# Optimization experiments

Hardware: AMD Instinct MI355X
Metric: run time of the kernel (lower is better)

Reference implementation:

```python
import jax, jax.numpy as jnp
import numpy as np

B, S, D_IN, D_OUT = 4, 2048, 1024, 1024

def setup_inputs() -> dict:
    key = jax.random.key(0)
    k_x, k_q, k_k, k_v = jax.random.split(key, 4)
    return {
        "x": jax.random.normal(k_x, (B, S, D_IN), dtype=jnp.float32),
        "W_query": jax.random.uniform(k_q, (D_IN, D_OUT), dtype=jnp.float32),
        "W_key": jax.random.uniform(k_k, (D_IN, D_OUT), dtype=jnp.float32),
        "W_value": jax.random.uniform(k_v, (D_IN, D_OUT), dtype=jnp.float32),
    }

def reference(x, W_query, W_key, W_value):
    seq_len = x.shape[1]
    d_out = W_key.shape[-1]
    # fused QKV projection: x @ concat([Wq, Wk, Wv], -1), then split
    qkv = x @ jnp.concatenate([W_query, W_key, W_value], axis=-1)  # [B,S,3*d_out]
    query, key, value = jnp.split(qkv, 3, axis=2)
    # raw scores [B,S,S]; causal mask applied BEFORE scaling (as in source)
    attn_weights = jnp.einsum("bqd,bkd->bqk", query, key)
    causal = jnp.triu(jnp.ones((seq_len, seq_len), dtype=bool), k=1)
    attn_weights = jnp.where(causal[None, :, :], -jnp.inf, attn_weights)
    scaled = attn_weights / jnp.asarray(d_out, x.dtype) ** 0.5
    attn_scores = jax.nn.softmax(scaled, axis=-1)  # dropout p=0 -> identity
    context_vectors = jnp.einsum("bqk,bkd->bqd", attn_scores, value)
    return (context_vectors, attn_scores)
```

## Files before the change

kernel.cpp:

```cpp
#include <hip/hip_runtime.h>
#include <cstdint>
#include <cstddef>


#define S_LEN 2048
#define D_DIM 1024
#define NBATCH 4
#define MEG (1024 * 1024)

typedef __attribute__((ext_vector_type(4))) float floatx4;
typedef __attribute__((ext_vector_type(8))) __bf16 bf16x8;
typedef __attribute__((ext_vector_type(8))) short short8v;

__device__ __forceinline__ unsigned short f2bf(float f) {
  union { float f; unsigned u; } v; v.f = f;
  unsigned r = v.u + 0x7FFF + ((v.u >> 16) & 1);
  return (unsigned short)(r >> 16);
}
__device__ __forceinline__ float bf2f(unsigned short h) {
  union { unsigned u; float f; } v; v.u = ((unsigned)h) << 16; return v.f;
}

__device__ __forceinline__ void async_copy16(const void* g, void* l) {
  __builtin_amdgcn_global_load_lds(
      (const __attribute__((address_space(1))) void*)g,
      (__attribute__((address_space(3))) void*)l, 16, 0, 0);
}

#define VMCNT0() asm volatile("s_waitcnt vmcnt(0)" ::: "memory")
#define RAW_BAR() __builtin_amdgcn_s_barrier()
#define MFMA_BF16 __builtin_amdgcn_mfma_f32_16x16x32_bf16


__device__ __forceinline__ void split_core8(
    const short* __restrict__ Ah, const short* __restrict__ Al,
    const short* __restrict__ Bh, const short* __restrict__ Bl,
    int lda, int ldb, int kIters, int blockM, int blockN,
    short (*AsH)[256][32], short (*AsL)[256][32],
    short (*BsH)[128][32], short (*BsL)[128][32],
    floatx4 (&acc)[4][4])
{
  const int tid  = threadIdx.x;
  const int lane = tid & 63;
  const int wave = tid >> 6;
  const int wm = (wave >> 1) * 64;
  const int wn = (wave & 1) * 64;
  const int fm = lane & 15;
  const int fu = lane >> 4;

  int rA[4], sA[4], rB[4], sB[4];
  #pragma unroll
  for (int i = 0; i < 4; ++i) {
    rA[i] = wm + i * 16 + fm;
    sA[i] = (fu ^ ((rA[i] >> 1) & 3)) * 8;
    rB[i] = wn + i * 16 + fm;
    sB[i] = (fu ^ ((rB[i] >> 1) & 3)) * 8;
  }

  floatx4 zero = {0.f, 0.f, 0.f, 0.f};
  #pragma unroll
  for (int i = 0; i < 4; ++i)
    #pragma unroll
    for (int j = 0; j < 4; ++j)
      acc[i][j] = zero;

  const int r0 = tid >> 2;
  const int u0 = tid & 3;
  const int su = (u0 ^ ((r0 >> 1) & 3)) * 8;
  const size_t a0 = (size_t)(blockM + r0) * lda + su;
  const size_t a1 = a0 + (size_t)128 * lda;
  const size_t b0 = (size_t)(blockN + r0) * ldb + su;

  auto stage0 = [&](int bf, int kb) {
    async_copy16(Ah + a0 + kb, &AsH[bf][r0][u0 * 8]);
    async_copy16(Al + a0 + kb, &AsL[bf][r0][u0 * 8]);
    async_copy16(Bh + b0 + kb, &BsH[bf][r0][u0 * 8]);
  };
  auto stage1 = [&](int bf, int kb) {
    async_copy16(Ah + a1 + kb, &AsH[bf][r0 + 128][u0 * 8]);
    async_copy16(Al + a1 + kb, &AsL[bf][r0 + 128][u0 * 8]);
    async_copy16(Bl + b0 + kb, &BsL[bf][r0][u0 * 8]);
  };

  stage0(0, 0);
  stage1(0, 0);
  VMCNT0();
  RAW_BAR();

  for (int kt = 0; kt < kIters; ++kt) {
    const int cur = kt & 1;
    const int kb = (kt + 1) * 32;
    const bool pf = (kt + 1) < kIters;

    bf16x8 bh[4], bl[4];
    #pragma unroll
    for (int j = 0; j < 4; ++j) {
      bh[j] = *(const bf16x8*)(&BsH[cur][rB[j]][sB[j]]);
      bl[j] = *(const bf16x8*)(&BsL[cur][rB[j]][sB[j]]);
    }
    bf16x8 ah0 = *(const bf16x8*)(&AsH[cur][rA[0]][sA[0]]);
    bf16x8 al0 = *(const bf16x8*)(&AsL[cur][rA[0]][sA[0]]);
    bf16x8 ah1 = *(const bf16x8*)(&AsH[cur][rA[1]][sA[1]]);
    bf16x8 al1 = *(const bf16x8*)(&AsL[cur][rA[1]][sA[1]]);
    if (pf) stage0(cur ^ 1, kb);
    RAW_BAR();
    __builtin_amdgcn_s_setprio(1);
    #pragma unroll
    for (int j = 0; j < 4; ++j) {
      acc[0][j] = MFMA_BF16(ah0, bh[j], acc[0][j], 0, 0, 0);
      acc[0][j] = MFMA_BF16(ah0, bl[j], acc[0][j], 0, 0, 0);
      acc[0][j] = MFMA_BF16(al0, bh[j], acc[0][j], 0, 0, 0);
      acc[1][j] = MFMA_BF16(ah1, bh[j], acc[1][j], 0, 0, 0);
      acc[1][j] = MFMA_BF16(ah1, bl[j], acc[1][j], 0, 0, 0);
      acc[1][j] = MFMA_BF16(al1, bh[j], acc[1][j], 0, 0, 0);
    }
    __builtin_amdgcn_s_setprio(0);
    RAW_BAR();

    bf16x8 ah2 = *(const bf16x8*)(&AsH[cur][rA[2]][sA[2]]);
    bf16x8 al2 = *(const bf16x8*)(&AsL[cur][rA[2]][sA[2]]);
    bf16x8 ah3 = *(const bf16x8*)(&AsH[cur][rA[3]][sA[3]]);
    bf16x8 al3 = *(const bf16x8*)(&AsL[cur][rA[3]][sA[3]]);
    if (pf) stage1(cur ^ 1, kb);
    RAW_BAR();
    __builtin_amdgcn_s_setprio(1);
    #pragma unroll
    for (int j = 0; j < 4; ++j) {
      acc[2][j] = MFMA_BF16(ah2, bh[j], acc[2][j], 0, 0, 0);
      acc[2][j] = MFMA_BF16(ah2, bl[j], acc[2][j], 0, 0, 0);
      acc[2][j] = MFMA_BF16(al2, bh[j], acc[2][j], 0, 0, 0);
      acc[3][j] = MFMA_BF16(ah3, bh[j], acc[3][j], 0, 0, 0);
      acc[3][j] = MFMA_BF16(ah3, bl[j], acc[3][j], 0, 0, 0);
      acc[3][j] = MFMA_BF16(al3, bh[j], acc[3][j], 0, 0, 0);
    }
    __builtin_amdgcn_s_setprio(0);
    VMCNT0();
    RAW_BAR();
  }
}

__device__ __forceinline__ void single_core8(
    const short* __restrict__ A, const short* __restrict__ B,
    int lda, int ldb, int kIters, int blockM, int blockN,
    short (*As)[256][32], short (*Bs)[128][32], floatx4 (&acc)[4][4])
{
  const int tid  = threadIdx.x;
  const int lane = tid & 63;
  const int wave = tid >> 6;
  const int wm = (wave >> 1) * 64;
  const int wn = (wave & 1) * 64;
  const int fm = lane & 15;
  const int fu = lane >> 4;

  int rA[4], sA[4], rB[4], sB[4];
  #pragma unroll
  for (int i = 0; i < 4; ++i) {
    rA[i] = wm + i * 16 + fm;
    sA[i] = (fu ^ ((rA[i] >> 1) & 3)) * 8;
    rB[i] = wn + i * 16 + fm;
    sB[i] = (fu ^ ((rB[i] >> 1) & 3)) * 8;
  }

  floatx4 zero = {0.f, 0.f, 0.f, 0.f};
  #pragma unroll
  for (int i = 0; i < 4; ++i)
    #pragma unroll
    for (int j = 0; j < 4; ++j)
      acc[i][j] = zero;

  const int r0 = tid >> 2;
  const int u0 = tid & 3;
  const int su = (u0 ^ ((r0 >> 1) & 3)) * 8;
  const size_t a0 = (size_t)(blockM + r0) * lda + su;
  const size_t a1 = a0 + (size_t)128 * lda;
  const size_t b0 = (size_t)(blockN + r0) * ldb + su;

  auto stage0 = [&](int bf, int kb) {
    async_copy16(A + a0 + kb, &As[bf][r0][u0 * 8]);
    async_copy16(B + b0 + kb, &Bs[bf][r0][u0 * 8]);
  };
  auto stage1 = [&](int bf, int kb) {
    async_copy16(A + a1 + kb, &As[bf][r0 + 128][u0 * 8]);
  };

  stage0(0, 0);
  stage1(0, 0);
  VMCNT0();
  RAW_BAR();

  for (int kt = 0; kt < kIters; ++kt) {
    const int cur = kt & 1;
    const int kb = (kt + 1) * 32;
    const bool pf = (kt + 1) < kIters;

    bf16x8 bfr[4];
    #pragma unroll
    for (int j = 0; j < 4; ++j)
      bfr[j] = *(const bf16x8*)(&Bs[cur][rB[j]][sB[j]]);
    bf16x8 a0f = *(const bf16x8*)(&As[cur][rA[0]][sA[0]]);
    bf16x8 a1f = *(const bf16x8*)(&As[cur][rA[1]][sA[1]]);
    if (pf) stage0(cur ^ 1, kb);
    RAW_BAR();
    __builtin_amdgcn_s_setprio(1);
    #pragma unroll
    for (int j = 0; j < 4; ++j) {
      acc[0][j] = MFMA_BF16(a0f, bfr[j], acc[0][j], 0, 0, 0);
      acc[1][j] = MFMA_BF16(a1f, bfr[j], acc[1][j], 0, 0, 0);
    }
    __builtin_amdgcn_s_setprio(0);
    RAW_BAR();

    bf16x8 a2f = *(const bf16x8*)(&As[cur][rA[2]][sA[2]]);
    bf16x8 a3f = *(const bf16x8*)(&As[cur][rA[3]][sA[3]]);
    if (pf) stage1(cur ^ 1, kb);
    RAW_BAR();
    __builtin_amdgcn_s_setprio(1);
    #pragma unroll
    for (int j = 0; j < 4; ++j) {
      acc[2][j] = MFMA_BF16(a2f, bfr[j], acc[2][j], 0, 0, 0);
      acc[3][j] = MFMA_BF16(a3f, bfr[j], acc[3][j], 0, 0, 0);
    }
    __builtin_amdgcn_s_setprio(0);
    VMCNT0();
    RAW_BAR();
  }
}


__global__ __launch_bounds__(256) void k_cvt_w(
    const float* __restrict__ wq, const float* __restrict__ wk,
    const float* __restrict__ wv,
    short* __restrict__ wqh, short* __restrict__ wql,
    short* __restrict__ wkh, short* __restrict__ wkl,
    short* __restrict__ wvt, float* __restrict__ muSum)
{
  const int bid = blockIdx.x;
  const int tid = threadIdx.x;
  if (bid < 1024) {
    const float4* src;
    short *dh, *dl;
    size_t idx;
    if (bid < 512) {
      idx = (size_t)bid * 256 + tid;
      src = (const float4*)wq; dh = wqh; dl = wql;
    } else {
      idx = (size_t)(bid - 512) * 256 + tid;
      src = (const float4*)wk; dh = wkh; dl = wkl;
    }
    const float4 u4 = src[idx * 2];
    const float4 w4 = src[idx * 2 + 1];
    float f[8] = {u4.x, u4.y, u4.z, u4.w, w4.x, w4.y, w4.z, w4.w};
    short8v oh, ol;
    #pragma unroll
    for (int e = 0; e < 8; ++e) {
      const unsigned short h = f2bf(f[e]);
      oh[e] = (short)h;
      ol[e] = (short)f2bf(f[e] - bf2f(h));
    }
    *(short8v*)(dh + idx * 8) = oh;
    *(short8v*)(dl + idx * 8) = ol;
  } else {
    if (bid == 1024) {
      float4 z = {0.f, 0.f, 0.f, 0.f};
      ((float4*)muSum)[tid] = z;
    }
    const int rem = bid - 1024;
    const int bx = rem & 31, by = rem >> 5;
    const int tx = tid & 31, ty = tid >> 5;
    __shared__ float tile[32][33];
    const int colIn = bx * 32 + tx;
    #pragma unroll
    for (int i = 0; i < 4; ++i) {
      const int rowIn = by * 32 + ty + i * 8;
      tile[ty + i * 8][tx] = wv[(size_t)rowIn * D_DIM + colIn];
    }
    __syncthreads();
    const int colOut = by * 32 + tx;
    #pragma unroll
    for (int i = 0; i < 4; ++i) {
      const int rowOut = bx * 32 + ty + i * 8;
      wvt[(size_t)rowOut * D_DIM + colOut] = (short)f2bf(tile[tx][ty + i * 8]);
    }
  }
}


__global__ __launch_bounds__(256) void k_m_cvtx(
    const short* __restrict__ wqh, const short* __restrict__ wql,
    const short* __restrict__ wkh, const short* __restrict__ wkl,
    short* __restrict__ mth, short* __restrict__ mtl,
    float* __restrict__ muSum,
    const float4* __restrict__ x,
    short* __restrict__ xh, short* __restrict__ xl)
{
  __shared__ alignas(16) short AsH[2][64][32];
  __shared__ alignas(16) short AsL[2][64][32];
  __shared__ alignas(16) short BsH[2][64][32];
  __shared__ alignas(16) short BsL[2][64][32];
  const int g = blockIdx.x;
  const int tid = threadIdx.x;

  if (g < 256) {
    floatx4 acc[2][2];
    const int blockM = (g >> 4) * 64;
    const int blockN = (g & 15) * 64;
    const int lane = tid & 63, wave = tid >> 6;
    const int wm = (wave >> 1) * 32, wn = (wave & 1) * 32;
    const int fm = lane & 15, fk = (lane >> 4) * 8;

    floatx4 zero = {0.f, 0.f, 0.f, 0.f};
    #pragma unroll
    for (int i = 0; i < 2; ++i)
      #pragma unroll
      for (int j = 0; j < 2; ++j)
        acc[i][j] = zero;

    const int sr = tid >> 2;
    const int sc = (tid & 3) * 8;
    const short* ah0 = wkh + (size_t)(blockM + sr) * D_DIM + sc;
    const short* al0 = wkl + (size_t)(blockM + sr) * D_DIM + sc;
    const short* bh0 = wqh + (size_t)(blockN + sr) * D_DIM + sc;
    const short* bl0 = wql + (size_t)(blockN + sr) * D_DIM + sc;
    short* ahB = &AsH[0][0][0]; short* alB = &AsL[0][0][0];
    short* bhB = &BsH[0][0][0]; short* blB = &BsL[0][0][0];
    const int l0 = tid * 8, l1 = (tid + 256) * 8;

    for (int kt = 0; kt < 16; ++kt) {
      const int kb = kt * 64;
      async_copy16(ah0 + kb, ahB + l0);
      async_copy16(ah0 + kb + 32, ahB + l1);
      async_copy16(al0 + kb, alB + l0);
      async_copy16(al0 + kb + 32, alB + l1);
      async_copy16(bh0 + kb, bhB + l0);
      async_copy16(bh0 + kb + 32, bhB + l1);
      async_copy16(bl0 + kb, blB + l0);
      async_copy16(bl0 + kb + 32, blB + l1);
      __syncthreads();
      #pragma unroll
      for (int ks = 0; ks < 2; ++ks) {
        bf16x8 ah[2], al[2], bh[2], bl[2];
        #pragma unroll
        for (int i = 0; i < 2; ++i) {
          ah[i] = *(const bf16x8*)(&AsH[ks][wm + i * 16 + fm][fk]);
          al[i] = *(const bf16x8*)(&AsL[ks][wm + i * 16 + fm][fk]);
        }
        #pragma unroll
        for (int j = 0; j < 2; ++j) {
          bh[j] = *(const bf16x8*)(&BsH[ks][wn + j * 16 + fm][fk]);
          bl[j] = *(const bf16x8*)(&BsL[ks][wn + j * 16 + fm][fk]);
        }
        #pragma unroll
        for (int i = 0; i < 2; ++i)
          #pragma unroll
          for (int j = 0; j < 2; ++j) {
            acc[i][j] = MFMA_BF16(ah[i], bh[j], acc[i][j], 0, 0, 0);
            acc[i][j] = MFMA_BF16(ah[i], bl[j], acc[i][j], 0, 0, 0);
            acc[i][j] = MFMA_BF16(al[i], bh[j], acc[i][j], 0, 0, 0);
          }
      }
      __syncthreads();
    }

    const int rb = wm + ((lane >> 4) << 2);
    const int cb = wn + (lane & 15);
    #pragma unroll
    for (int i = 0; i < 2; ++i)
      #pragma unroll
      for (int j = 0; j < 2; ++j) {
        const int n = blockN + cb + j * 16;
        #pragma unroll
        for (int r = 0; r < 2 * 2; ++r) {
          const int m = blockM + rb + i * 16 + r;
          const float f = acc[i][j][r];
          const unsigned short h = f2bf(f);
          mth[(size_t)m * D_DIM + n] = (short)h;
          mtl[(size_t)m * D_DIM + n] = (short)f2bf(f - bf2f(h));
        }
      }
    #pragma unroll
    for (int i = 0; i < 2; ++i)
      #pragma unroll
      for (int r = 0; r < 4; ++r) {
        float v = acc[i][0][r] + acc[i][1][r];
        v += __shfl_xor(v, 1); v += __shfl_xor(v, 2);
        v += __shfl_xor(v, 4); v += __shfl_xor(v, 8);
        if ((lane & 15) == 0)
          atomicAdd(&muSum[blockM + rb + i * 16 + r], v);
      }
  } else {
    const size_t idx = (size_t)(g - 256) * 256 + tid;
    const float4 u4 = x[idx * 2];
    const float4 w4 = x[idx * 2 + 1];
    float f[8] = {u4.x, u4.y, u4.z, u4.w, w4.x, w4.y, w4.z, w4.w};
    short8v oh, ol;
    #pragma unroll
    for (int e = 0; e < 8; ++e) {
      const unsigned short h = f2bf(f[e]);
      oh[e] = (short)h;
      ol[e] = (short)f2bf(f[e] - bf2f(h));
    }
    *(short8v*)(xh + idx * 8) = oh;
    *(short8v*)(xl + idx * 8) = ol;
  }
}


__global__ __launch_bounds__(256) void k_rowstats(
    const short* __restrict__ xh, const short* __restrict__ xl,
    const float* __restrict__ muSum, float* __restrict__ sq, float* __restrict__ u)
{
  const int r = blockIdx.x, tid = threadIdx.x;
  const ushort4 h = *(const ushort4*)(xh + (size_t)r * D_DIM + tid * 4);
  const ushort4 l = *(const ushort4*)(xl + (size_t)r * D_DIM + tid * 4);
  const float4 m4 = *(const float4*)(muSum + tid * 4);
  const float x0 = bf2f(h.x) + bf2f(l.x);
  const float x1 = bf2f(h.y) + bf2f(l.y);
  const float x2 = bf2f(h.z) + bf2f(l.z);
  const float x3 = bf2f(h.w) + bf2f(l.w);
  float s = x0 + x1 + x2 + x3;
  float uu = m4.x * x0 + m4.y * x1 + m4.z * x2 + m4.w * x3;
  #pragma unroll
  for (int off = 32; off > 0; off >>= 1) {
    s  += __shfl_xor(s, off);
    uu += __shfl_xor(uu, off);
  }
  __shared__ float ps[4], pu[4];
  if ((tid & 63) == 0) { ps[tid >> 6] = s; pu[tid >> 6] = uu; }
  __syncthreads();
  if (tid == 0) {
    sq[r] = ps[0] + ps[1] + ps[2] + ps[3];
    u[r]  = (pu[0] + pu[1] + pu[2] + pu[3]) * (1.0f / 1024.0f);
  }
}


__global__ __launch_bounds__(512) void k_gemm_n8(
    const short* __restrict__ xh, const short* __restrict__ xl,
    const short* __restrict__ mth, const short* __restrict__ mtl,
    const float* __restrict__ sq, const float* __restrict__ muSum,
    short* __restrict__ nh, short* __restrict__ nl)
{
  __shared__ alignas(16) short AsH[2][256][32];
  __shared__ alignas(16) short AsL[2][256][32];
  __shared__ alignas(16) short BsH[2][128][32];
  __shared__ alignas(16) short BsL[2][128][32];
  floatx4 acc[4][4];
  const int g = blockIdx.x;
  const int swz = (g & 7) * 32 + (g >> 3);
  const int blockM = (swz >> 3) * 256;
  const int blockN = (swz & 7) * 128;
  split_core8(xh, xl, mth, mtl, D_DIM, D_DIM, D_DIM / 32,
              blockM, blockN, AsH, AsL, BsH, BsL, acc);

  const int tid = threadIdx.x, lane = tid & 63, wave = tid >> 6;
  const int wm = (wave >> 1) * 64, wn = (wave & 1) * 64;
  const int rb = wm + ((lane >> 4) << 2);
  const int cb = wn + (lane & 15);
  #pragma unroll
  for (int i = 0; i < 4; ++i)
    #pragma unroll
    for (int j = 0; j < 4; ++j) {
      const int n = blockN + cb + j * 16;
      const float muv = muSum[n] * (1.0f / 1024.0f);
      #pragma unroll
      for (int r = 0; r < 4; ++r) {
        const int m = blockM + rb + i * 16 + r;
        const float f = acc[i][j][r] - sq[m] * muv;
        const unsigned short h = f2bf(f);
        nh[(size_t)m * D_DIM + n] = (short)h;
        nl[(size_t)m * D_DIM + n] = (short)f2bf(f - bf2f(h));
      }
    }
}


__global__ __launch_bounds__(512) void k_gemm_sv8(
    const short* __restrict__ nh, const short* __restrict__ nl,
    const short* __restrict__ xh, const short* __restrict__ xl,
    const float* __restrict__ sq, const float* __restrict__ u,
    const short* __restrict__ wvt, float* __restrict__ attn,
    short* __restrict__ vt)
{
  __shared__ alignas(16) short AsH[2][256][32];
  __shared__ alignas(16) short AsL[2][256][32];
  __shared__ alignas(16) short BsH[2][128][32];
  __shared__ alignas(16) short BsL[2][128][32];
  floatx4 acc[4][4];

  const int g = blockIdx.x;
  const int tid = threadIdx.x, lane = tid & 63, wave = tid >> 6;
  const int wm = (wave >> 1) * 64, wn = (wave & 1) * 64;
  const int rb = wm + ((lane >> 4) << 2);
  const int cb = wn + (lane & 15);

  if (g < 288) {
    const int item = (g & 7) * 36 + (g >> 3);
    const int b = item / 72;
    int t = item - b * 72;
    int bi = 0;
    while (t >= 2 * bi + 2) { t -= 2 * bi + 2; ++bi; }
    const int bj = t;

    const size_t boff = (size_t)b * S_LEN * D_DIM;
    split_core8(nh + boff, nl + boff, xh + boff, xl + boff,
                D_DIM, D_DIM, D_DIM / 32, bi * 256, bj * 128,
                AsH, AsL, BsH, BsL, acc);

    float* out = attn + (size_t)b * S_LEN * S_LEN;
    const int rowBase = (b << 11) + bi * 256;
    const int colBase = (b << 11) + bj * 128;
    #pragma unroll
    for (int j = 0; j < 4; ++j) {
      const int n = bj * 128 + cb + j * 16;
      const float uv = u[colBase + cb + j * 16];
      #pragma unroll
      for (int i = 0; i < 4; ++i)
        #pragma unroll
        for (int r = 0; r < 4; ++r) {
          const int m = bi * 256 + rb + i * 16 + r;
          const float sv = sq[rowBase + rb + i * 16 + r];
          out[(size_t)m * S_LEN + n] = acc[i][j][r] + sv * uv;
        }
    }
  } else {
    const int vb = g - 288;
    const int blockM = (vb >> 3) * 256;
    const int blockN = (vb & 7) * 128;
    single_core8(xh, wvt, D_DIM, D_DIM, D_DIM / 32, blockM, blockN,
                 AsH, BsH, acc);
    #pragma unroll
    for (int i = 0; i < 4; ++i)
      #pragma unroll
      for (int j = 0; j < 4; ++j) {
        const int n = blockN + cb + j * 16;
        const int m0 = blockM + rb + i * 16;
        const int b = m0 >> 11;
        const int s0 = m0 & (S_LEN - 1);
        ushort4 pk;
        pk.x = f2bf(acc[i][j][0]); pk.y = f2bf(acc[i][j][1]);
        pk.z = f2bf(acc[i][j][2]); pk.w = f2bf(acc[i][j][3]);
        *(ushort4*)(vt + ((size_t)b * D_DIM + n) * S_LEN + s0) = pk;
      }
  }
}


__global__ __launch_bounds__(256) void k_softmax(float* __restrict__ attn,
                                                 short* __restrict__ pb) {
  const int b = blockIdx.x >> 11;
  const int q = blockIdx.x & (S_LEN - 1);
  float* row  = attn + ((size_t)b * S_LEN + q) * S_LEN;
  short* prow = pb   + ((size_t)b * S_LEN + q) * S_LEN;
  const int tid = threadIdx.x;
  const int k0 = tid * 8;
  const int kBand = ((q >> 7) + 1) << 7;
  __shared__ float sMax[4], sSum[4];

  float v[8];
  if (k0 <= q) {
    const float4 a0 = *(const float4*)(row + k0);
    const float4 a1 = *(const float4*)(row + k0 + 4);
    v[0] = a0.x; v[1] = a0.y; v[2] = a0.z; v[3] = a0.w;
    v[4] = a1.x; v[5] = a1.y; v[6] = a1.z; v[7] = a1.w;
  } else {
    #pragma unroll
    for (int e = 0; e < 8; ++e) v[e] = -3.0e38f;
  }

  float mx = -3.0e38f;
  #pragma unroll
  for (int e = 0; e < 8; ++e) {
    v[e] = (k0 + e <= q) ? v[e] : -3.0e38f;
    mx = fmaxf(mx, v[e]);
  }
  #pragma unroll
  for (int off = 32; off > 0; off >>= 1) mx = fmaxf(mx, __shfl_xor(mx, off));
  if ((tid & 63) == 0) sMax[tid >> 6] = mx;
  __syncthreads();
  mx = fmaxf(fmaxf(sMax[0], sMax[1]), fmaxf(sMax[2], sMax[3]));

  float s = 0.f;
  #pragma unroll
  for (int e = 0; e < 8; ++e) {
    const float p = (k0 + e <= q) ? __expf((v[e] - mx) * 0.03125f) : 0.f;
    v[e] = p;
    s += p;
  }
  #pragma unroll
  for (int off = 32; off > 0; off >>= 1) s += __shfl_xor(s, off);
  if ((tid & 63) == 0) sSum[tid >> 6] = s;
  __syncthreads();
  s = sSum[0] + sSum[1] + sSum[2] + sSum[3];
  const float inv = 1.0f / s;

  float o[8];
  #pragma unroll
  for (int e = 0; e < 8; ++e) o[e] = v[e] * inv;
  float4 w0 = {o[0], o[1], o[2], o[3]};
  float4 w1 = {o[4], o[5], o[6], o[7]};
  *(float4*)(row + k0) = w0;
  *(float4*)(row + k0 + 4) = w1;
  if (k0 < kBand) {
    ushort4 p0, p1;
    p0.x = f2bf(o[0]); p0.y = f2bf(o[1]); p0.z = f2bf(o[2]); p0.w = f2bf(o[3]);
    p1.x = f2bf(o[4]); p1.y = f2bf(o[5]); p1.z = f2bf(o[6]); p1.w = f2bf(o[7]);
    *(ushort4*)(prow + k0) = p0;
    *(ushort4*)(prow + k0 + 4) = p1;
  }
}


__global__ __launch_bounds__(256) void k_gemm_ctx(
    const short* __restrict__ pb, const short* __restrict__ vt,
    float* __restrict__ ctx)
{
  __shared__ alignas(16) short As2[2][128][32];
  __shared__ alignas(16) short Bs2[2][128][32];
  floatx4 acc[4][4];
  const int b = blockIdx.z;
  const int by = 15 - blockIdx.y;
  const int blockM = by * 128;
  const int blockN = blockIdx.x * 128;
  const int kIters = (by + 1) * 2;
  const short* A = pb + (size_t)b * S_LEN * S_LEN;
  const short* B = vt + (size_t)b * D_DIM * S_LEN;

  const int tid = threadIdx.x, lane = tid & 63, wave = tid >> 6;
  const int wm = (wave >> 1) * 64, wn = (wave & 1) * 64;
  const int fm = lane & 15, fk = (lane >> 4) * 8;
  const int r0 = tid >> 2, c0 = (tid & 3) * 8;

  floatx4 zero = {0.f, 0.f, 0.f, 0.f};
  #pragma unroll
  for (int i = 0; i < 4; ++i)
    #pragma unroll
    for (int j = 0; j < 4; ++j)
      acc[i][j] = zero;

  const short* a0 = A + (size_t)(blockM + r0) * S_LEN + c0;
  const short* a1 = a0 + (size_t)64 * S_LEN;
  const short* b0 = B + (size_t)(blockN + r0) * S_LEN + c0;
  const short* b1 = b0 + (size_t)64 * S_LEN;
  short* asBase = &As2[0][0][0];
  short* bsBase = &Bs2[0][0][0];
  short* as0 = asBase + (size_t)tid * 8;
  short* as1 = asBase + (size_t)(tid + 256) * 8;
  short* as2 = asBase + (size_t)(tid + 512) * 8;
  short* as3 = asBase + (size_t)(tid + 768) * 8;
  short* bs0 = bsBase + (size_t)tid * 8;
  short* bs1 = bsBase + (size_t)(tid + 256) * 8;
  short* bs2 = bsBase + (size_t)(tid + 512) * 8;
  short* bs3 = bsBase + (size_t)(tid + 768) * 8;

  for (int kt = 0; kt < kIters; ++kt) {
    const int kb = kt * 64;
    async_copy16(a0 + kb, as0);
    async_copy16(a1 + kb, as1);
    async_copy16(a0 + kb + 32, as2);
    async_copy16(a1 + kb + 32, as3);
    async_copy16(b0 + kb, bs0);
    async_copy16(b1 + kb, bs1);
    async_copy16(b0 + kb + 32, bs2);
    async_copy16(b1 + kb + 32, bs3);
    __syncthreads();
    #pragma unroll
    for (int ks = 0; ks < 2; ++ks) {
      bf16x8 af[4], bfr[4];
      #pragma unroll
      for (int i = 0; i < 4; ++i)
        af[i] = *(const bf16x8*)(&As2[ks][wm + i * 16 + fm][fk]);
      #pragma unroll
      for (int j = 0; j < 4; ++j)
        bfr[j] = *(const bf16x8*)(&Bs2[ks][wn + j * 16 + fm][fk]);
      #pragma unroll
      for (int i = 0; i < 4; ++i)
        #pragma unroll
        for (int j = 0; j < 4; ++j)
          acc[i][j] = MFMA_BF16(af[i], bfr[j], acc[i][j], 0, 0, 0);
    }
    __syncthreads();
  }

  float* out = ctx + (size_t)b * S_LEN * D_DIM;
  const int rb = wm + ((lane >> 4) << 2);
  const int cb = wn + (lane & 15);
  #pragma unroll
  for (int i = 0; i < 4; ++i)
    #pragma unroll
    for (int j = 0; j < 4; ++j) {
      const int n = blockN + cb + j * 16;
      #pragma unroll
      for (int r = 0; r < 4; ++r) {
        const int m = blockM + rb + i * 16 + r;
        out[(size_t)m * D_DIM + n] = acc[i][j][r];
      }
    }
}


extern "C" void kernel_launch(void* const* d_in, const int* in_sizes, int n_in,
                              void* d_out, int out_size, void* d_ws, size_t ws_size,
                              hipStream_t stream) {
  const float* x  = (const float*)d_in[0];
  const float* wq = (const float*)d_in[1];
  const float* wk = (const float*)d_in[2];
  const float* wv = (const float*)d_in[3];

  float* out  = (float*)d_out;
  float* ctx  = out;
  float* attn = out + (size_t)NBATCH * S_LEN * D_DIM;

  short* ws  = (short*)d_ws;
  short* xh  = ws;
  short* xl  = xh + (size_t)8 * MEG;
  short* wqh = xl + (size_t)8 * MEG;
  short* wql = wqh + (size_t)1 * MEG;
  short* wkh = wql + (size_t)1 * MEG;
  short* wkl = wkh + (size_t)1 * MEG;
  short* wvt = wkl + (size_t)1 * MEG;
  short* mth = wvt + (size_t)1 * MEG;
  short* mtl = mth + (size_t)1 * MEG;
  short* nh  = mtl + (size_t)1 * MEG;
  short* nl  = nh + (size_t)8 * MEG;
  short* vt  = nl + (size_t)8 * MEG;
  short* pb  = nh;
  float* fb  = (float*)(vt + (size_t)8 * MEG);
  float* muS = fb;
  float* sq  = fb + 1024;
  float* u   = sq + 8192;

  k_cvt_w<<<2048, 256, 0, stream>>>(wq, wk, wv, wqh, wql, wkh, wkl, wvt, muS);
  k_m_cvtx<<<4352, 256, 0, stream>>>(wqh, wql, wkh, wkl, mth, mtl, muS,
                                     (const float4*)x, xh, xl);
  k_rowstats<<<8192, 256, 0, stream>>>(xh, xl, muS, sq, u);
  k_gemm_n8<<<256, 512, 0, stream>>>(xh, xl, mth, mtl, sq, muS, nh, nl);
  k_gemm_sv8<<<544, 512, 0, stream>>>(nh, nl, xh, xl, sq, u, wvt, attn, vt);
  k_softmax<<<NBATCH * S_LEN, 256, 0, stream>>>(attn, pb);
  k_gemm_ctx<<<dim3(8, 16, 4), 256, 0, stream>>>(pb, vt, ctx);
}
```

Baseline: 366.2 us.

## Triple-buffer LDS tiles in GEMM cores with prefetch depth two

Both GEMM core loops (split and single precision) move from double to triple buffering. Two k-tiles are prefetched ahead, and the end-of-iteration wait becomes a partial vmcnt wait instead of draining all global-to-LDS loads. The goal is to hide more global memory latency behind the MFMA work. In exchange, LDS use per block rises by half in the split kernels. Any other caller of single_core8 whose buffers are not resized to three would index out of bounds.

```diff
diff --git a/kernel.cpp b/kernel.cpp
--- a/kernel.cpp
+++ b/kernel.cpp
@@ -28,6 +28,8 @@
 }
 
 #define VMCNT0() asm volatile("s_waitcnt vmcnt(0)" ::: "memory")
+#define VMCNT3() asm volatile("s_waitcnt vmcnt(3)" ::: "memory")
+#define VMCNT6() asm volatile("s_waitcnt vmcnt(6)" ::: "memory")
 #define RAW_BAR() __builtin_amdgcn_s_barrier()
 #define MFMA_BF16 __builtin_amdgcn_mfma_f32_16x16x32_bf16
 
@@ -84,13 +86,17 @@
 
   stage0(0, 0);
   stage1(0, 0);
-  VMCNT0();
+  stage0(1, 32);
+  stage1(1, 32);
+  VMCNT6();
   RAW_BAR();
 
+  int cur = 0;
   for (int kt = 0; kt < kIters; ++kt) {
-    const int cur = kt & 1;
-    const int kb = (kt + 1) * 32;
-    const bool pf = (kt + 1) < kIters;
+    const int pf2 = kt + 2;
+    const bool pf = pf2 < kIters;
+    const int pbuf = cur >= 1 ? cur - 1 : 2;
+    const int kb = pf2 * 32;
 
     bf16x8 bh[4], bl[4];
     #pragma unroll
@@ -102,7 +108,7 @@
     bf16x8 al0 = *(const bf16x8*)(&AsL[cur][rA[0]][sA[0]]);
     bf16x8 ah1 = *(const bf16x8*)(&AsH[cur][rA[1]][sA[1]]);
     bf16x8 al1 = *(const bf16x8*)(&AsL[cur][rA[1]][sA[1]]);
-    if (pf) stage0(cur ^ 1, kb);
+    if (pf) stage0(pbuf, kb);
     RAW_BAR();
     __builtin_amdgcn_s_setprio(1);
     #pragma unroll
@@ -121,7 +127,7 @@
     bf16x8 al2 = *(const bf16x8*)(&AsL[cur][rA[2]][sA[2]]);
     bf16x8 ah3 = *(const bf16x8*)(&AsH[cur][rA[3]][sA[3]]);
     bf16x8 al3 = *(const bf16x8*)(&AsL[cur][rA[3]][sA[3]]);
-    if (pf) stage1(cur ^ 1, kb);
+    if (pf) stage1(pbuf, kb);
     RAW_BAR();
     __builtin_amdgcn_s_setprio(1);
     #pragma unroll
@@ -134,8 +140,9 @@
       acc[3][j] = MFMA_BF16(al3, bh[j], acc[3][j], 0, 0, 0);
     }
     __builtin_amdgcn_s_setprio(0);
-    VMCNT0();
+    if (pf) { VMCNT6(); } else { VMCNT0(); }
     RAW_BAR();
+    cur = (cur == 2) ? 0 : cur + 1;
   }
 }
 
@@ -185,13 +192,17 @@
 
   stage0(0, 0);
   stage1(0, 0);
-  VMCNT0();
+  stage0(1, 32);
+  stage1(1, 32);
+  VMCNT3();
   RAW_BAR();
 
+  int cur = 0;
   for (int kt = 0; kt < kIters; ++kt) {
-    const int cur = kt & 1;
-    const int kb = (kt + 1) * 32;
-    const bool pf = (kt + 1) < kIters;
+    const int pf2 = kt + 2;
+    const bool pf = pf2 < kIters;
+    const int pbuf = cur >= 1 ? cur - 1 : 2;
+    const int kb = pf2 * 32;
 
     bf16x8 bfr[4];
     #pragma unroll
@@ -199,7 +210,7 @@
       bfr[j] = *(const bf16x8*)(&Bs[cur][rB[j]][sB[j]]);
     bf16x8 a0f = *(const bf16x8*)(&As[cur][rA[0]][sA[0]]);
     bf16x8 a1f = *(const bf16x8*)(&As[cur][rA[1]][sA[1]]);
-    if (pf) stage0(cur ^ 1, kb);
+    if (pf) stage0(pbuf, kb);
     RAW_BAR();
     __builtin_amdgcn_s_setprio(1);
     #pragma unroll
@@ -212,7 +223,7 @@
 
     bf16x8 a2f = *(const bf16x8*)(&As[cur][rA[2]][sA[2]]);
     bf16x8 a3f = *(const bf16x8*)(&As[cur][rA[3]][sA[3]]);
-    if (pf) stage1(cur ^ 1, kb);
+    if (pf) stage1(pbuf, kb);
     RAW_BAR();
     __builtin_amdgcn_s_setprio(1);
     #pragma unroll
@@ -221,8 +232,9 @@
       acc[3][j] = MFMA_BF16(a3f, bfr[j], acc[3][j], 0, 0, 0);
     }
     __builtin_amdgcn_s_setprio(0);
-    VMCNT0();
+    if (pf) { VMCNT3(); } else { VMCNT0(); }
     RAW_BAR();
+    cur = (cur == 2) ? 0 : cur + 1;
   }
 }
 
@@ -440,10 +452,10 @@
     const float* __restrict__ sq, const float* __restrict__ muSum,
     short* __restrict__ nh, short* __restrict__ nl)
 {
-  __shared__ alignas(16) short AsH[2][256][32];
-  __shared__ alignas(16) short AsL[2][256][32];
-  __shared__ alignas(16) short BsH[2][128][32];
-  __shared__ alignas(16) short BsL[2][128][32];
+  __shared__ alignas(16) short AsH[3][256][32];
+  __shared__ alignas(16) short AsL[3][256][32];
+  __shared__ alignas(16) short BsH[3][128][32];
+  __shared__ alignas(16) short BsL[3][128][32];
   floatx4 acc[4][4];
   const int g = blockIdx.x;
   const int swz = (g & 7) * 32 + (g >> 3);
@@ -481,10 +493,10 @@
     const short* __restrict__ wvt, float* __restrict__ attn,
     short* __restrict__ vt)
 {
-  __shared__ alignas(16) short AsH[2][256][32];
-  __shared__ alignas(16) short AsL[2][256][32];
-  __shared__ alignas(16) short BsH[2][128][32];
-  __shared__ alignas(16) short BsL[2][128][32];
+  __shared__ alignas(16) short AsH[3][256][32];
+  __shared__ alignas(16) short AsL[3][256][32];
+  __shared__ alignas(16) short BsH[3][128][32];
+  __shared__ alignas(16) short BsL[3][128][32];
   floatx4 acc[4][4];
 
   const int g = blockIdx.x;
```

Result: no change. 367.9 us (+0.5%).

## Restructure GEMM cores into register-double-buffered pipeline with one barrier per k-step

Applied to the files above, without the earlier changes.

Both GEMM inner loops now prefetch two k-tiles ahead into LDS and preload the next tile's fragments into a second register set while the current tile's MFMAs run. This cuts the barriers per iteration from four to one and overlaps LDS reads with matrix math. In exchange it doubles fragment register usage, which may lower occupancy or cause spills. The loop is unrolled by two and assumes an even kIters, and the prefetch into buffer kt&1 relies on that buffer's fragments already having been read into registers before the barrier.

```diff
diff --git a/kernel.cpp b/kernel.cpp
--- a/kernel.cpp
+++ b/kernel.cpp
@@ -28,6 +28,9 @@
 }
 
 #define VMCNT0() asm volatile("s_waitcnt vmcnt(0)" ::: "memory")
+#define VMCNT6() asm volatile("s_waitcnt vmcnt(6)" ::: "memory")
+#define VMCNT3() asm volatile("s_waitcnt vmcnt(3)" ::: "memory")
+#define LGKM0()  asm volatile("s_waitcnt lgkmcnt(0)" ::: "memory")
 #define RAW_BAR() __builtin_amdgcn_s_barrier()
 #define MFMA_BF16 __builtin_amdgcn_mfma_f32_16x16x32_bf16
 
@@ -71,71 +74,67 @@
   const size_t a1 = a0 + (size_t)128 * lda;
   const size_t b0 = (size_t)(blockN + r0) * ldb + su;
 
-  auto stage0 = [&](int bf, int kb) {
+  auto stage = [&](int bf, int kb) {
     async_copy16(Ah + a0 + kb, &AsH[bf][r0][u0 * 8]);
     async_copy16(Al + a0 + kb, &AsL[bf][r0][u0 * 8]);
     async_copy16(Bh + b0 + kb, &BsH[bf][r0][u0 * 8]);
-  };
-  auto stage1 = [&](int bf, int kb) {
     async_copy16(Ah + a1 + kb, &AsH[bf][r0 + 128][u0 * 8]);
     async_copy16(Al + a1 + kb, &AsL[bf][r0 + 128][u0 * 8]);
     async_copy16(Bl + b0 + kb, &BsL[bf][r0][u0 * 8]);
   };
 
-  stage0(0, 0);
-  stage1(0, 0);
+  bf16x8 A0h[4], A0l[4], B0h[4], B0l[4];
+  bf16x8 A1h[4], A1l[4], B1h[4], B1l[4];
+
+  stage(0, 0);
+  stage(1, 32);
+  VMCNT6();
+  RAW_BAR();
+  #pragma unroll
+  for (int j = 0; j < 4; ++j) {
+    B0h[j] = *(const bf16x8*)(&BsH[0][rB[j]][sB[j]]);
+    B0l[j] = *(const bf16x8*)(&BsL[0][rB[j]][sB[j]]);
+    A0h[j] = *(const bf16x8*)(&AsH[0][rA[j]][sA[j]]);
+    A0l[j] = *(const bf16x8*)(&AsL[0][rA[j]][sA[j]]);
+  }
+  LGKM0();
   VMCNT0();
   RAW_BAR();
 
-  for (int kt = 0; kt < kIters; ++kt) {
-    const int cur = kt & 1;
-    const int kb = (kt + 1) * 32;
-    const bool pf = (kt + 1) < kIters;
-
-    bf16x8 bh[4], bl[4];
-    #pragma unroll
-    for (int j = 0; j < 4; ++j) {
-      bh[j] = *(const bf16x8*)(&BsH[cur][rB[j]][sB[j]]);
-      bl[j] = *(const bf16x8*)(&BsL[cur][rB[j]][sB[j]]);
-    }
-    bf16x8 ah0 = *(const bf16x8*)(&AsH[cur][rA[0]][sA[0]]);
-    bf16x8 al0 = *(const bf16x8*)(&AsL[cur][rA[0]][sA[0]]);
-    bf16x8 ah1 = *(const bf16x8*)(&AsH[cur][rA[1]][sA[1]]);
-    bf16x8 al1 = *(const bf16x8*)(&AsL[cur][rA[1]][sA[1]]);
-    if (pf) stage0(cur ^ 1, kb);
-    RAW_BAR();
+  auto iterf = [&](int kt,
+                   bf16x8 (&cAh)[4], bf16x8 (&cAl)[4],
+                   bf16x8 (&cBh)[4], bf16x8 (&cBl)[4],
+                   bf16x8 (&nAh)[4], bf16x8 (&nAl)[4],
+                   bf16x8 (&nBh)[4], bf16x8 (&nBl)[4]) {
+    const int nbuf = (kt + 1) & 1;
+    if (kt + 2 < kIters) stage(kt & 1, (kt + 2) * 32);
+    if (kt + 1 < kIters) {
+      #pragma unroll
+      for (int j = 0; j < 4; ++j) {
+        nBh[j] = *(const bf16x8*)(&BsH[nbuf][rB[j]][sB[j]]);
+        nBl[j] = *(const bf16x8*)(&BsL[nbuf][rB[j]][sB[j]]);
+        nAh[j] = *(const bf16x8*)(&AsH[nbuf][rA[j]][sA[j]]);
+        nAl[j] = *(const bf16x8*)(&AsL[nbuf][rA[j]][sA[j]]);
+      }
+    }
     __builtin_amdgcn_s_setprio(1);
     #pragma unroll
-    for (int j = 0; j < 4; ++j) {
-      acc[0][j] = MFMA_BF16(ah0, bh[j], acc[0][j], 0, 0, 0);
-      acc[0][j] = MFMA_BF16(ah0, bl[j], acc[0][j], 0, 0, 0);
-      acc[0][j] = MFMA_BF16(al0, bh[j], acc[0][j], 0, 0, 0);
-      acc[1][j] = MFMA_BF16(ah1, bh[j], acc[1][j], 0, 0, 0);
-      acc[1][j] = MFMA_BF16(ah1, bl[j], acc[1][j], 0, 0, 0);
-      acc[1][j] = MFMA_BF16(al1, bh[j], acc[1][j], 0, 0, 0);
-    }
+    for (int i = 0; i < 4; ++i)
+      #pragma unroll
+      for (int j = 0; j < 4; ++j) {
+        acc[i][j] = MFMA_BF16(cAh[i], cBh[j], acc[i][j], 0, 0, 0);
+        acc[i][j] = MFMA_BF16(cAh[i], cBl[j], acc[i][j], 0, 0, 0);
+        acc[i][j] = MFMA_BF16(cAl[i], cBh[j], acc[i][j], 0, 0, 0);
+      }
     __builtin_amdgcn_s_setprio(0);
-    RAW_BAR();
-
-    bf16x8 ah2 = *(const bf16x8*)(&AsH[cur][rA[2]][sA[2]]);
-    bf16x8 al2 = *(const bf16x8*)(&AsL[cur][rA[2]][sA[2]]);
-    bf16x8 ah3 = *(const bf16x8*)(&AsH[cur][rA[3]][sA[3]]);
-    bf16x8 al3 = *(const bf16x8*)(&AsL[cur][rA[3]][sA[3]]);
-    if (pf) stage1(cur ^ 1, kb);
-    RAW_BAR();
-    __builtin_amdgcn_s_setprio(1);
-    #pragma unroll
-    for (int j = 0; j < 4; ++j) {
-      acc[2][j] = MFMA_BF16(ah2, bh[j], acc[2][j], 0, 0, 0);
-      acc[2][j] = MFMA_BF16(ah2, bl[j], acc[2][j], 0, 0, 0);
-      acc[2][j] = MFMA_BF16(al2, bh[j], acc[2][j], 0, 0, 0);
-      acc[3][j] = MFMA_BF16(ah3, bh[j], acc[3][j], 0, 0, 0);
-      acc[3][j] = MFMA_BF16(ah3, bl[j], acc[3][j], 0, 0, 0);
-      acc[3][j] = MFMA_BF16(al3, bh[j], acc[3][j], 0, 0, 0);
-    }
-    __builtin_amdgcn_s_setprio(0);
+    LGKM0();
     VMCNT0();
     RAW_BAR();
+  };
+
+  for (int kt = 0; kt < kIters; kt += 2) {
+    iterf(kt,     A0h, A0l, B0h, B0l, A1h, A1l, B1h, B1l);
+    iterf(kt + 1, A1h, A1l, B1h, B1l, A0h, A0l, B0h, B0l);
   }
 }
 
@@ -175,54 +174,54 @@
   const size_t a1 = a0 + (size_t)128 * lda;
   const size_t b0 = (size_t)(blockN + r0) * ldb + su;
 
-  auto stage0 = [&](int bf, int kb) {
+  auto stage = [&](int bf, int kb) {
     async_copy16(A + a0 + kb, &As[bf][r0][u0 * 8]);
     async_copy16(B + b0 + kb, &Bs[bf][r0][u0 * 8]);
-  };
-  auto stage1 = [&](int bf, int kb) {
     async_copy16(A + a1 + kb, &As[bf][r0 + 128][u0 * 8]);
   };
 
-  stage0(0, 0);
-  stage1(0, 0);
+  bf16x8 A0f[4], B0f[4], A1f[4], B1f[4];
+
+  stage(0, 0);
+  stage(1, 32);
+  VMCNT3();
+  RAW_BAR();
+  #pragma unroll
+  for (int j = 0; j < 4; ++j) {
+    B0f[j] = *(const bf16x8*)(&Bs[0][rB[j]][sB[j]]);
+    A0f[j] = *(const bf16x8*)(&As[0][rA[j]][sA[j]]);
+  }
+  LGKM0();
   VMCNT0();
   RAW_BAR();
 
-  for (int kt = 0; kt < kIters; ++kt) {
-    const int cur = kt & 1;
-    const int kb = (kt + 1) * 32;
-    const bool pf = (kt + 1) < kIters;
-
-    bf16x8 bfr[4];
-    #pragma unroll
-    for (int j = 0; j < 4; ++j)
-      bfr[j] = *(const bf16x8*)(&Bs[cur][rB[j]][sB[j]]);
-    bf16x8 a0f = *(const bf16x8*)(&As[cur][rA[0]][sA[0]]);
-    bf16x8 a1f = *(const bf16x8*)(&As[cur][rA[1]][sA[1]]);
-    if (pf) stage0(cur ^ 1, kb);
-    RAW_BAR();
+  auto iterf = [&](int kt,
+                   bf16x8 (&cAf)[4], bf16x8 (&cBf)[4],
+                   bf16x8 (&nAf)[4], bf16x8 (&nBf)[4]) {
+    const int nbuf = (kt + 1) & 1;
+    if (kt + 2 < kIters) stage(kt & 1, (kt + 2) * 32);
+    if (kt + 1 < kIters) {
+      #pragma unroll
+      for (int j = 0; j < 4; ++j) {
+        nBf[j] = *(const bf16x8*)(&Bs[nbuf][rB[j]][sB[j]]);
+        nAf[j] = *(const bf16x8*)(&As[nbuf][rA[j]][sA[j]]);
+      }
+    }
     __builtin_amdgcn_s_setprio(1);
     #pragma unroll
-    for (int j = 0; j < 4; ++j) {
-      acc[0][j] = MFMA_BF16(a0f, bfr[j], acc[0][j], 0, 0, 0);
-      acc[1][j] = MFMA_BF16(a1f, bfr[j], acc[1][j], 0, 0, 0);
-    }
+    for (int i = 0; i < 4; ++i)
+      #pragma unroll
+      for (int j = 0; j < 4; ++j)
+        acc[i][j] = MFMA_BF16(cAf[i], cBf[j], acc[i][j], 0, 0, 0);
     __builtin_amdgcn_s_setprio(0);
-    RAW_BAR();
-
-    bf16x8 a2f = *(const bf16x8*)(&As[cur][rA[2]][sA[2]]);
-    bf16x8 a3f = *(const bf16x8*)(&As[cur][rA[3]][sA[3]]);
-    if (pf) stage1(cur ^ 1, kb);
-    RAW_BAR();
-    __builtin_amdgcn_s_setprio(1);
-    #pragma unroll
-    for (int j = 0; j < 4; ++j) {
-      acc[2][j] = MFMA_BF16(a2f, bfr[j], acc[2][j], 0, 0, 0);
-      acc[3][j] = MFMA_BF16(a3f, bfr[j], acc[3][j], 0, 0, 0);
-    }
-    __builtin_amdgcn_s_setprio(0);
+    LGKM0();
     VMCNT0();
     RAW_BAR();
+  };
+
+  for (int kt = 0; kt < kIters; kt += 2) {
+    iterf(kt,     A0f, B0f, A1f, B1f);
+    iterf(kt + 1, A1f, B1f, A0f, B0f);
   }
 }
 
```

New measurement: 378.5 us. 1.03x slower.
